# Performance work log

Measured on AMD Instinct MI355X. Metric: run time of the kernel, lower is better.

## Reference

```python
import jax, jax.numpy as jnp
import numpy as np

N_NODES = 100000
N_EDGES = 1600000
IN_F = 32
D = 128
OUT = 16


def setup_inputs() -> dict:
    key = jax.random.key(0)
    ks = jax.random.split(key, 12)
    inp = {
        "x": jax.random.normal(ks[0], (N_NODES, IN_F), dtype=jnp.float32),
        "edge_index": jax.random.randint(ks[1], (2, N_EDGES), 0, N_NODES, dtype=jnp.int64),
        # node embedder (Linear IN_F -> D)
        "W_emb": jax.random.normal(ks[2], (IN_F, D), dtype=jnp.float32) / np.sqrt(IN_F),
        "b_emb": jnp.zeros((D,), dtype=jnp.float32),
        # conv1: relation weight, root weight, bias
        "W1_rel": jax.random.normal(ks[3], (D, D), dtype=jnp.float32) / np.sqrt(D),
        "W1_root": jax.random.normal(ks[4], (D, D), dtype=jnp.float32) / np.sqrt(D),
        "b1": jnp.zeros((D,), dtype=jnp.float32),
        # conv2
        "W2_rel": jax.random.normal(ks[5], (D, D), dtype=jnp.float32) / np.sqrt(D),
        "W2_root": jax.random.normal(ks[6], (D, D), dtype=jnp.float32) / np.sqrt(D),
        "b2": jnp.zeros((D,), dtype=jnp.float32),
        # final layer D -> OUT
        "W_out": jax.random.normal(ks[7], (D, OUT), dtype=jnp.float32) / np.sqrt(D),
        "b_out": jnp.zeros((OUT,), dtype=jnp.float32),
    }
    return inp


def _rgcn_mean(h, src, dst, W_rel, W_root, b):
    # FastRGCNConv with num_relations=1, aggr='mean':
    # out_i = mean_{j -> i}(h_j @ W_rel) + h_i @ W_root + b
    msg = h[src] @ W_rel  # [E, D] gather + per-edge transform
    agg = jax.ops.segment_sum(msg, dst, num_segments=N_NODES)
    cnt = jax.ops.segment_sum(jnp.ones((dst.shape[0],), dtype=h.dtype), dst,
                              num_segments=N_NODES)
    agg = agg / jnp.maximum(cnt, 1.0)[:, None]  # scatter-mean; isolated nodes -> 0
    return agg + h @ W_root + b


def reference(x, edge_index, W_emb, b_emb, W1_rel, W1_root, b1,
              W2_rel, W2_root, b2, W_out, b_out):
    src, dst = edge_index[0], edge_index[1]
    h = x @ W_emb + b_emb                                   # node embed
    h = jax.nn.relu(_rgcn_mean(h, src, dst, W1_rel, W1_root, b1))
    h = jax.nn.relu(_rgcn_mean(h, src, dst, W2_rel, W2_root, b2))
    return h @ W_out + b_out                                # [N_NODES, OUT]
```

## Files before the change

### kernel.cpp

```cpp
#include <hip/hip_runtime.h>
#include <hip/hip_bf16.h>

#define N_NODES 100000
#define N_EDGES 1600000
#define IN_F    32
#define D       128
#define OUT_F   16
#define NB      ((N_NODES + 255) / 256)
#define NSLICE  8
#define SLICE_NODES (N_NODES / NSLICE)
#define FILL_CHUNKS 512

typedef __attribute__((ext_vector_type(8))) short  bf16x8;
typedef __attribute__((ext_vector_type(4))) float  f32x4;

__device__ __forceinline__ unsigned short f2bf(float x) {
    unsigned u = __float_as_uint(x);
    unsigned r = (u + 0x7FFFu + ((u >> 16) & 1u)) >> 16;
    return (unsigned short)r;
}
__device__ __forceinline__ float bf2f(unsigned short h) {
    return __uint_as_float(((unsigned)h) << 16);
}

__global__ __launch_bounds__(256) void k_embed(const float* __restrict__ x,
                                               const float* __restrict__ W,
                                               const float* __restrict__ b,
                                               unsigned short* __restrict__ h_hi,
                                               unsigned short* __restrict__ h_lo) {
    __shared__ float xs[2][IN_F];
    const int col = threadIdx.x & 127;
    const int ng  = threadIdx.x >> 7;
    const int node = blockIdx.x * 2 + ng;

    if (threadIdx.x < 64) {
        int r = threadIdx.x >> 5, c = threadIdx.x & 31;
        int n2 = blockIdx.x * 2 + r;
        xs[r][c] = (n2 < N_NODES) ? x[(long)n2 * IN_F + c] : 0.f;
    }
    __syncthreads();
    if (node >= N_NODES) return;

    float acc = b[col];
#pragma unroll
    for (int k = 0; k < IN_F; ++k)
        acc += xs[ng][k] * W[k * D + col];
    unsigned short hi = f2bf(acc);
    h_hi[(long)node * D + col] = hi;
    h_lo[(long)node * D + col] = f2bf(acc - bf2f(hi));
}

__global__ __launch_bounds__(256) void k_count(const int* __restrict__ dst,
                                               int* __restrict__ cnt) {
    const int slice = blockIdx.x & (NSLICE - 1);
    const int chunk = blockIdx.x >> 3;
    const int lo = slice * SLICE_NODES;
    const int hi = lo + SLICE_NODES;
    for (int e = chunk * 256 + threadIdx.x; e < N_EDGES; e += FILL_CHUNKS * 256) {
        int d = dst[e];
        if (d >= lo && d < hi) atomicAdd(&cnt[d], 1);
    }
}

__global__ __launch_bounds__(256) void k_scan1(const int* __restrict__ cnt,
                                               int* __restrict__ part,
                                               int* __restrict__ blockSums) {
    __shared__ int s[256];
    int i = blockIdx.x * 256 + threadIdx.x;
    int v = (i < N_NODES) ? cnt[i] : 0;
    s[threadIdx.x] = v;
    __syncthreads();
    for (int off = 1; off < 256; off <<= 1) {
        int x = (threadIdx.x >= off) ? s[threadIdx.x - off] : 0;
        __syncthreads();
        s[threadIdx.x] += x;
        __syncthreads();
    }
    if (i < N_NODES) part[i] = s[threadIdx.x] - v;
    if (threadIdx.x == 255) blockSums[blockIdx.x] = s[255];
}

__global__ __launch_bounds__(512) void k_scan2(int* __restrict__ blockSums) {
    __shared__ int s[512];
    int t = threadIdx.x;
    int v = (t < NB) ? blockSums[t] : 0;
    s[t] = v;
    __syncthreads();
    for (int off = 1; off < 512; off <<= 1) {
        int x = (t >= off) ? s[t - off] : 0;
        __syncthreads();
        s[t] += x;
        __syncthreads();
    }
    if (t < NB) blockSums[t] = s[t] - v;
}

__global__ __launch_bounds__(256) void k_scan3(int* __restrict__ offsets,
                                               const int* __restrict__ blockSums,
                                               int* __restrict__ cursor) {
    int i = blockIdx.x * 256 + threadIdx.x;
    if (i < N_NODES) {
        int o = offsets[i] + blockSums[blockIdx.x];
        offsets[i] = o;
        cursor[i]  = o;
    }
}

__global__ __launch_bounds__(256) void k_fill(const int* __restrict__ src,
                                              const int* __restrict__ dst,
                                              int* __restrict__ cursor,
                                              int* __restrict__ csr) {
    const int slice = blockIdx.x & (NSLICE - 1);
    const int chunk = blockIdx.x >> 3;
    const int lo = slice * SLICE_NODES;
    const int hi = lo + SLICE_NODES;
    for (int e = chunk * 256 + threadIdx.x; e < N_EDGES; e += FILL_CHUNKS * 256) {
        int d = dst[e];
        if (d >= lo && d < hi) {
            int p = atomicAdd(&cursor[d], 1);
            csr[p] = src[e];
        }
    }
}

__global__ __launch_bounds__(256) void k_gather(const unsigned short* __restrict__ h_hi,
                                                const int* __restrict__ csr,
                                                const int* __restrict__ offsets,
                                                const int* __restrict__ cnt,
                                                unsigned short* __restrict__ ag_hi,
                                                unsigned short* __restrict__ ag_lo) {
    const int node = blockIdx.x * 16 + (threadIdx.x >> 4);
    const int q8 = (threadIdx.x & 15) << 3;

    const int beg = offsets[node];
    const int deg = cnt[node];
    const int end = beg + deg;

    float a0[8], a1[8];
#pragma unroll
    for (int j = 0; j < 8; ++j) { a0[j] = 0.f; a1[j] = 0.f; }

    int i = beg;
    for (; i + 3 < end; i += 4) {
        int s0 = csr[i], s1 = csr[i + 1], s2 = csr[i + 2], s3 = csr[i + 3];
        bf16x8 v0 = *reinterpret_cast<const bf16x8*>(h_hi + (long)s0 * D + q8);
        bf16x8 v1 = *reinterpret_cast<const bf16x8*>(h_hi + (long)s1 * D + q8);
        bf16x8 v2 = *reinterpret_cast<const bf16x8*>(h_hi + (long)s2 * D + q8);
        bf16x8 v3 = *reinterpret_cast<const bf16x8*>(h_hi + (long)s3 * D + q8);
#pragma unroll
        for (int j = 0; j < 8; ++j) {
            a0[j] += bf2f((unsigned short)v0[j]) + bf2f((unsigned short)v1[j]);
            a1[j] += bf2f((unsigned short)v2[j]) + bf2f((unsigned short)v3[j]);
        }
    }
    for (; i < end; ++i) {
        int s0 = csr[i];
        bf16x8 v0 = *reinterpret_cast<const bf16x8*>(h_hi + (long)s0 * D + q8);
#pragma unroll
        for (int j = 0; j < 8; ++j) a0[j] += bf2f((unsigned short)v0[j]);
    }

    const float sc = 1.f / fmaxf((float)deg, 1.f);
    unsigned short hh[8], ll[8];
#pragma unroll
    for (int j = 0; j < 8; ++j) {
        float v = (a0[j] + a1[j]) * sc;
        unsigned short h = f2bf(v);
        hh[j] = h;
        ll[j] = f2bf(v - bf2f(h));
    }
    *reinterpret_cast<bf16x8*>(ag_hi + (long)node * D + q8) = *reinterpret_cast<bf16x8*>(hh);
    *reinterpret_cast<bf16x8*>(ag_lo + (long)node * D + q8) = *reinterpret_cast<bf16x8*>(ll);
}

__global__ __launch_bounds__(256) void k_wprep(const float* __restrict__ W1r,
                                               const float* __restrict__ W1o,
                                               const float* __restrict__ W2r,
                                               const float* __restrict__ W2o,
                                               unsigned short* __restrict__ wp) {
    int c = blockIdx.x * 256 + threadIdx.x;
    int layer = c >> 12;
    int ko = (c >> 7) & 31;
    int n = c & 127;
    const float* Wrel  = layer ? W2r : W1r;
    const float* Wroot = layer ? W2o : W1o;

    unsigned short hi[8], lo[8];
#pragma unroll
    for (int j = 0; j < 8; ++j) {
        int k = ko * 8 + j;
        float w = (k < D) ? Wrel[k * D + n] : Wroot[(k - D) * D + n];
        unsigned short h = f2bf(w);
        hi[j] = h;
        lo[j] = f2bf(w - bf2f(h));
    }
    unsigned short* base = wp + layer * 65536 + ((ko * 128 + n) << 3);
    *reinterpret_cast<bf16x8*>(base)         = *reinterpret_cast<bf16x8*>(hi);
    *reinterpret_cast<bf16x8*>(base + 32768) = *reinterpret_cast<bf16x8*>(lo);
}

__global__ __launch_bounds__(256) void k_transform(const unsigned short* __restrict__ agg_hi,
                                                   const unsigned short* __restrict__ agg_lo,
                                                   const unsigned short* __restrict__ hin_hi,
                                                   const unsigned short* __restrict__ hin_lo,
                                                   const unsigned short* __restrict__ Wh,
                                                   const unsigned short* __restrict__ Wl,
                                                   const float* __restrict__ b,
                                                   unsigned short* __restrict__ ho_hi,
                                                   unsigned short* __restrict__ ho_lo) {
    __shared__ unsigned short Ahi[32 * 32 * 8];
    __shared__ unsigned short Alo[32 * 32 * 8];
    const int base = blockIdx.x * 32;

    for (int it = 0; it < 4; ++it) {
        int c  = it * 256 + threadIdx.x;
        int ko = c & 31;
        int row = c >> 5;
        long node = base + row;
        long off = (ko < 16) ? (node * D + ko * 8) : (node * D + (ko - 16) * 8);
        const unsigned short* ph = (ko < 16) ? agg_hi : hin_hi;
        const unsigned short* pl = (ko < 16) ? agg_lo : hin_lo;
        bf16x8 vh = *reinterpret_cast<const bf16x8*>(ph + off);
        bf16x8 vl = *reinterpret_cast<const bf16x8*>(pl + off);
        int byteoff = ((ko * 32 + row) * 16) ^ ((ko & 7) << 4);
        *reinterpret_cast<bf16x8*>(reinterpret_cast<char*>(Ahi) + byteoff) = vh;
        *reinterpret_cast<bf16x8*>(reinterpret_cast<char*>(Alo) + byteoff) = vl;
    }
    __syncthreads();

    const int lane = threadIdx.x & 63;
    const int wid  = threadIdx.x >> 6;
    const int mw = wid & 1;
    const int nw = wid >> 1;
    const int l15 = lane & 15;
    const int l4  = lane >> 4;

    f32x4 acc[4];
#pragma unroll
    for (int ct = 0; ct < 4; ++ct) acc[ct] = (f32x4){0.f, 0.f, 0.f, 0.f};

    const int arow = mw * 16 + l15;

#pragma unroll
    for (int s = 0; s < 8; ++s) {
        const int ks = s * 4 + l4;
        const int abyte = ((ks * 32 + arow) * 16) ^ ((ks & 7) << 4);
        bf16x8 ah = *reinterpret_cast<const bf16x8*>(
                        reinterpret_cast<const char*>(Ahi) + abyte);
        bf16x8 al = *reinterpret_cast<const bf16x8*>(
                        reinterpret_cast<const char*>(Alo) + abyte);
#pragma unroll
        for (int ct = 0; ct < 4; ++ct) {
            const int colb = nw * 64 + ct * 16 + l15;
            const long bidx = ((long)(ks * 128 + colb)) << 3;
            bf16x8 bh = *reinterpret_cast<const bf16x8*>(Wh + bidx);
            bf16x8 bl = *reinterpret_cast<const bf16x8*>(Wl + bidx);
            acc[ct] = __builtin_amdgcn_mfma_f32_16x16x32_bf16(ah, bh, acc[ct], 0, 0, 0);
            acc[ct] = __builtin_amdgcn_mfma_f32_16x16x32_bf16(al, bh, acc[ct], 0, 0, 0);
            acc[ct] = __builtin_amdgcn_mfma_f32_16x16x32_bf16(ah, bl, acc[ct], 0, 0, 0);
        }
    }

#pragma unroll
    for (int ct = 0; ct < 4; ++ct) {
        const int col = nw * 64 + ct * 16 + l15;
        const float bv = b[col];
#pragma unroll
        for (int r = 0; r < 4; ++r) {
            long node = base + mw * 16 + l4 * 4 + r;
            float v = fmaxf(acc[ct][r] + bv, 0.f);
            unsigned short h = f2bf(v);
            ho_hi[node * D + col] = h;
            ho_lo[node * D + col] = f2bf(v - bf2f(h));
        }
    }
}

__global__ __launch_bounds__(256) void k_out(const unsigned short* __restrict__ h_hi,
                                             const unsigned short* __restrict__ h_lo,
                                             const float* __restrict__ W,
                                             const float* __restrict__ b,
                                             float* __restrict__ out) {
    long t = (long)blockIdx.x * 256 + threadIdx.x;
    if (t >= (long)N_NODES * OUT_F) return;
    int n = (int)(t >> 4);
    int o = (int)t & 15;
    const unsigned short* hh = h_hi + (long)n * D;
    const unsigned short* hl = h_lo + (long)n * D;
    float acc = b[o];
#pragma unroll
    for (int k = 0; k < D; k += 8) {
        bf16x8 vh = *reinterpret_cast<const bf16x8*>(hh + k);
        bf16x8 vl = *reinterpret_cast<const bf16x8*>(hl + k);
#pragma unroll
        for (int j = 0; j < 8; ++j) {
            float v = bf2f((unsigned short)vh[j]) + bf2f((unsigned short)vl[j]);
            acc += v * W[(k + j) * OUT_F + o];
        }
    }
    out[t] = acc;
}

extern "C" void kernel_launch(void* const* d_in, const int* in_sizes, int n_in,
                              void* d_out, int out_size, void* d_ws, size_t ws_size,
                              hipStream_t stream) {
    const float* x      = (const float*)d_in[0];
    const int*   edge   = (const int*)d_in[1];
    const float* W_emb  = (const float*)d_in[2];
    const float* b_emb  = (const float*)d_in[3];
    const float* W1_rel = (const float*)d_in[4];
    const float* W1_root= (const float*)d_in[5];
    const float* b1     = (const float*)d_in[6];
    const float* W2_rel = (const float*)d_in[7];
    const float* W2_root= (const float*)d_in[8];
    const float* b2     = (const float*)d_in[9];
    const float* W_out  = (const float*)d_in[10];
    const float* b_out  = (const float*)d_in[11];
    float* out = (float*)d_out;

    const int* src = edge;
    const int* dst = edge + N_EDGES;

    const size_t ND = (size_t)N_NODES * D;

    unsigned short* hA_hi = (unsigned short*)d_ws;
    unsigned short* hA_lo = hA_hi + ND;
    unsigned short* hB_hi = hA_lo + ND;
    unsigned short* hB_lo = hB_hi + ND;
    unsigned short* ag_hi = hB_lo + ND;
    unsigned short* ag_lo = ag_hi + ND;
    int*   cnt     = (int*)(ag_lo + ND);
    int*   offsets = cnt + N_NODES;
    int*   cursor  = offsets + N_NODES;
    int*   bsums   = cursor + N_NODES;
    unsigned short* wpack = (unsigned short*)(bsums + 400);
    int*   csr     = (int*)(wpack + 4 * 32768);

    hipMemsetAsync(cnt, 0, N_NODES * sizeof(int), stream);
    k_count<<<NSLICE * FILL_CHUNKS, 256, 0, stream>>>(dst, cnt);
    k_scan1<<<NB, 256, 0, stream>>>(cnt, offsets, bsums);
    k_scan2<<<1, 512, 0, stream>>>(bsums);
    k_scan3<<<NB, 256, 0, stream>>>(offsets, bsums, cursor);
    k_fill<<<NSLICE * FILL_CHUNKS, 256, 0, stream>>>(src, dst, cursor, csr);
    k_wprep<<<32, 256, 0, stream>>>(W1_rel, W1_root, W2_rel, W2_root, wpack);

    k_embed<<<(N_NODES + 1) / 2, 256, 0, stream>>>(x, W_emb, b_emb, hA_hi, hA_lo);

    k_gather<<<N_NODES / 16, 256, 0, stream>>>(hA_hi, csr, offsets, cnt, ag_hi, ag_lo);
    k_transform<<<N_NODES / 32, 256, 0, stream>>>(ag_hi, ag_lo, hA_hi, hA_lo,
                                                  wpack, wpack + 32768, b1, hB_hi, hB_lo);

    k_gather<<<N_NODES / 16, 256, 0, stream>>>(hB_hi, csr, offsets, cnt, ag_hi, ag_lo);
    k_transform<<<N_NODES / 32, 256, 0, stream>>>(ag_hi, ag_lo, hB_hi, hB_lo,
                                                  wpack + 65536, wpack + 98304, b2, hA_hi, hA_lo);

    k_out<<<((long)N_NODES * OUT_F + 255) / 256, 256, 0, stream>>>(hA_hi, hA_lo, W_out, b_out, out);
}
```

Before: 550.9 us.

## Fuse neighbor gather into transform and final projection into last layer

The separate gather kernel is merged into the MFMA transform kernel, so the mean-aggregated rows go straight into shared memory instead of a round trip through global ag_hi/ag_lo buffers. The last layer also applies the output projection in-kernel from shared memory, which removes the k_out launch and the write and re-read of the final hidden state. The embed kernel is rewritten to handle 16 nodes per block with vectorized loads and stores. The trade-off is that the fused kernel has fewer blocks (N/32 instead of N/16 for the gather part), and the latency of the irregular gather now sits inside the GEMM blocks, which could lower occupancy and overlap.

Measured after the change: 505.0 us. 8.3% less time.

```diff
diff --git a/kernel.cpp b/kernel.cpp
--- a/kernel.cpp
+++ b/kernel.cpp
@@ -28,26 +28,45 @@
                                                const float* __restrict__ b,
                                                unsigned short* __restrict__ h_hi,
                                                unsigned short* __restrict__ h_lo) {
-    __shared__ float xs[2][IN_F];
-    const int col = threadIdx.x & 127;
-    const int ng  = threadIdx.x >> 7;
-    const int node = blockIdx.x * 2 + ng;
-
-    if (threadIdx.x < 64) {
-        int r = threadIdx.x >> 5, c = threadIdx.x & 31;
-        int n2 = blockIdx.x * 2 + r;
-        xs[r][c] = (n2 < N_NODES) ? x[(long)n2 * IN_F + c] : 0.f;
+    __shared__ float xs[16][IN_F];
+    const int base = blockIdx.x * 16;
+
+    if (threadIdx.x < 128) {
+        int r = threadIdx.x >> 3, c4 = (threadIdx.x & 7) << 2;
+        *reinterpret_cast<float4*>(&xs[r][c4]) =
+            *reinterpret_cast<const float4*>(x + (long)(base + r) * IN_F + c4);
     }
     __syncthreads();
-    if (node >= N_NODES) return;
-
-    float acc = b[col];
-#pragma unroll
-    for (int k = 0; k < IN_F; ++k)
-        acc += xs[ng][k] * W[k * D + col];
-    unsigned short hi = f2bf(acc);
-    h_hi[(long)node * D + col] = hi;
-    h_lo[(long)node * D + col] = f2bf(acc - bf2f(hi));
+
+    const int nl   = threadIdx.x >> 4;
+    const int col0 = (threadIdx.x & 15) << 3;
+
+    float acc[8];
+    {
+        float4 b0 = *reinterpret_cast<const float4*>(b + col0);
+        float4 b1 = *reinterpret_cast<const float4*>(b + col0 + 4);
+        acc[0] = b0.x; acc[1] = b0.y; acc[2] = b0.z; acc[3] = b0.w;
+        acc[4] = b1.x; acc[5] = b1.y; acc[6] = b1.z; acc[7] = b1.w;
+    }
+#pragma unroll
+    for (int k = 0; k < IN_F; ++k) {
+        const float xv = xs[nl][k];
+        float4 w0 = *reinterpret_cast<const float4*>(W + k * D + col0);
+        float4 w1 = *reinterpret_cast<const float4*>(W + k * D + col0 + 4);
+        acc[0] += xv * w0.x; acc[1] += xv * w0.y; acc[2] += xv * w0.z; acc[3] += xv * w0.w;
+        acc[4] += xv * w1.x; acc[5] += xv * w1.y; acc[6] += xv * w1.z; acc[7] += xv * w1.w;
+    }
+
+    unsigned short hh[8], ll[8];
+#pragma unroll
+    for (int j = 0; j < 8; ++j) {
+        unsigned short h = f2bf(acc[j]);
+        hh[j] = h;
+        ll[j] = f2bf(acc[j] - bf2f(h));
+    }
+    long off = (long)(base + nl) * D + col0;
+    *reinterpret_cast<bf16x8*>(h_hi + off) = *reinterpret_cast<bf16x8*>(hh);
+    *reinterpret_cast<bf16x8*>(h_lo + off) = *reinterpret_cast<bf16x8*>(ll);
 }
 
 __global__ __launch_bounds__(256) void k_count(const int* __restrict__ dst,
@@ -123,56 +142,6 @@
     }
 }
 
-__global__ __launch_bounds__(256) void k_gather(const unsigned short* __restrict__ h_hi,
-                                                const int* __restrict__ csr,
-                                                const int* __restrict__ offsets,
-                                                const int* __restrict__ cnt,
-                                                unsigned short* __restrict__ ag_hi,
-                                                unsigned short* __restrict__ ag_lo) {
-    const int node = blockIdx.x * 16 + (threadIdx.x >> 4);
-    const int q8 = (threadIdx.x & 15) << 3;
-
-    const int beg = offsets[node];
-    const int deg = cnt[node];
-    const int end = beg + deg;
-
-    float a0[8], a1[8];
-#pragma unroll
-    for (int j = 0; j < 8; ++j) { a0[j] = 0.f; a1[j] = 0.f; }
-
-    int i = beg;
-    for (; i + 3 < end; i += 4) {
-        int s0 = csr[i], s1 = csr[i + 1], s2 = csr[i + 2], s3 = csr[i + 3];
-        bf16x8 v0 = *reinterpret_cast<const bf16x8*>(h_hi + (long)s0 * D + q8);
-        bf16x8 v1 = *reinterpret_cast<const bf16x8*>(h_hi + (long)s1 * D + q8);
-        bf16x8 v2 = *reinterpret_cast<const bf16x8*>(h_hi + (long)s2 * D + q8);
-        bf16x8 v3 = *reinterpret_cast<const bf16x8*>(h_hi + (long)s3 * D + q8);
-#pragma unroll
-        for (int j = 0; j < 8; ++j) {
-            a0[j] += bf2f((unsigned short)v0[j]) + bf2f((unsigned short)v1[j]);
-            a1[j] += bf2f((unsigned short)v2[j]) + bf2f((unsigned short)v3[j]);
-        }
-    }
-    for (; i < end; ++i) {
-        int s0 = csr[i];
-        bf16x8 v0 = *reinterpret_cast<const bf16x8*>(h_hi + (long)s0 * D + q8);
-#pragma unroll
-        for (int j = 0; j < 8; ++j) a0[j] += bf2f((unsigned short)v0[j]);
-    }
-
-    const float sc = 1.f / fmaxf((float)deg, 1.f);
-    unsigned short hh[8], ll[8];
-#pragma unroll
-    for (int j = 0; j < 8; ++j) {
-        float v = (a0[j] + a1[j]) * sc;
-        unsigned short h = f2bf(v);
-        hh[j] = h;
-        ll[j] = f2bf(v - bf2f(h));
-    }
-    *reinterpret_cast<bf16x8*>(ag_hi + (long)node * D + q8) = *reinterpret_cast<bf16x8*>(hh);
-    *reinterpret_cast<bf16x8*>(ag_lo + (long)node * D + q8) = *reinterpret_cast<bf16x8*>(ll);
-}
-
 __global__ __launch_bounds__(256) void k_wprep(const float* __restrict__ W1r,
                                                const float* __restrict__ W1o,
                                                const float* __restrict__ W2r,
@@ -199,37 +168,92 @@
     *reinterpret_cast<bf16x8*>(base + 32768) = *reinterpret_cast<bf16x8*>(lo);
 }
 
-__global__ __launch_bounds__(256) void k_transform(const unsigned short* __restrict__ agg_hi,
-                                                   const unsigned short* __restrict__ agg_lo,
-                                                   const unsigned short* __restrict__ hin_hi,
-                                                   const unsigned short* __restrict__ hin_lo,
-                                                   const unsigned short* __restrict__ Wh,
-                                                   const unsigned short* __restrict__ Wl,
-                                                   const float* __restrict__ b,
-                                                   unsigned short* __restrict__ ho_hi,
-                                                   unsigned short* __restrict__ ho_lo) {
+template <bool LAST>
+__global__ __launch_bounds__(256) void k_fused(const unsigned short* __restrict__ hin_hi,
+                                               const unsigned short* __restrict__ hin_lo,
+                                               const int* __restrict__ csr,
+                                               const int* __restrict__ offsets,
+                                               const int* __restrict__ cnt,
+                                               const unsigned short* __restrict__ Wh,
+                                               const unsigned short* __restrict__ Wl,
+                                               const float* __restrict__ b,
+                                               unsigned short* __restrict__ ho_hi,
+                                               unsigned short* __restrict__ ho_lo,
+                                               const float* __restrict__ Wout,
+                                               const float* __restrict__ bout,
+                                               float* __restrict__ outp) {
     __shared__ unsigned short Ahi[32 * 32 * 8];
     __shared__ unsigned short Alo[32 * 32 * 8];
     const int base = blockIdx.x * 32;
-
-    for (int it = 0; it < 4; ++it) {
-        int c  = it * 256 + threadIdx.x;
-        int ko = c & 31;
-        int row = c >> 5;
-        long node = base + row;
-        long off = (ko < 16) ? (node * D + ko * 8) : (node * D + (ko - 16) * 8);
-        const unsigned short* ph = (ko < 16) ? agg_hi : hin_hi;
-        const unsigned short* pl = (ko < 16) ? agg_lo : hin_lo;
-        bf16x8 vh = *reinterpret_cast<const bf16x8*>(ph + off);
-        bf16x8 vl = *reinterpret_cast<const bf16x8*>(pl + off);
+    const int tid  = threadIdx.x;
+
+    {
+        const int ko = tid & 15;
+        const int q8 = ko << 3;
+        for (int half = 0; half < 2; ++half) {
+            const int row  = half * 16 + (tid >> 4);
+            const int node = base + row;
+            const int beg = offsets[node];
+            const int deg = cnt[node];
+            const int end = beg + deg;
+
+            float a0[8], a1[8];
+#pragma unroll
+            for (int j = 0; j < 8; ++j) { a0[j] = 0.f; a1[j] = 0.f; }
+
+            int i = beg;
+            for (; i + 3 < end; i += 4) {
+                int s0 = csr[i], s1 = csr[i + 1], s2 = csr[i + 2], s3 = csr[i + 3];
+                bf16x8 v0 = *reinterpret_cast<const bf16x8*>(hin_hi + (long)s0 * D + q8);
+                bf16x8 v1 = *reinterpret_cast<const bf16x8*>(hin_hi + (long)s1 * D + q8);
+                bf16x8 v2 = *reinterpret_cast<const bf16x8*>(hin_hi + (long)s2 * D + q8);
+                bf16x8 v3 = *reinterpret_cast<const bf16x8*>(hin_hi + (long)s3 * D + q8);
+#pragma unroll
+                for (int j = 0; j < 8; ++j) {
+                    a0[j] += bf2f((unsigned short)v0[j]) + bf2f((unsigned short)v1[j]);
+                    a1[j] += bf2f((unsigned short)v2[j]) + bf2f((unsigned short)v3[j]);
+                }
+            }
+            for (; i < end; ++i) {
+                int s0 = csr[i];
+                bf16x8 v0 = *reinterpret_cast<const bf16x8*>(hin_hi + (long)s0 * D + q8);
+#pragma unroll
+                for (int j = 0; j < 8; ++j) a0[j] += bf2f((unsigned short)v0[j]);
+            }
+
+            const float sc = 1.f / fmaxf((float)deg, 1.f);
+            unsigned short hh[8], ll[8];
+#pragma unroll
+            for (int j = 0; j < 8; ++j) {
+                float v = (a0[j] + a1[j]) * sc;
+                unsigned short h = f2bf(v);
+                hh[j] = h;
+                ll[j] = f2bf(v - bf2f(h));
+            }
+            const int byteoff = ((ko * 32 + row) * 16) ^ ((ko & 7) << 4);
+            *reinterpret_cast<bf16x8*>(reinterpret_cast<char*>(Ahi) + byteoff) =
+                *reinterpret_cast<bf16x8*>(hh);
+            *reinterpret_cast<bf16x8*>(reinterpret_cast<char*>(Alo) + byteoff) =
+                *reinterpret_cast<bf16x8*>(ll);
+        }
+    }
+
+    for (int it = 0; it < 2; ++it) {
+        int c = it * 256 + tid;
+        int ko16 = c & 15;
+        int row  = c >> 4;
+        long off = (long)(base + row) * D + ko16 * 8;
+        bf16x8 vh = *reinterpret_cast<const bf16x8*>(hin_hi + off);
+        bf16x8 vl = *reinterpret_cast<const bf16x8*>(hin_lo + off);
+        int ko = 16 + ko16;
         int byteoff = ((ko * 32 + row) * 16) ^ ((ko & 7) << 4);
         *reinterpret_cast<bf16x8*>(reinterpret_cast<char*>(Ahi) + byteoff) = vh;
         *reinterpret_cast<bf16x8*>(reinterpret_cast<char*>(Alo) + byteoff) = vl;
     }
     __syncthreads();
 
-    const int lane = threadIdx.x & 63;
-    const int wid  = threadIdx.x >> 6;
+    const int lane = tid & 63;
+    const int wid  = tid >> 6;
     const int mw = wid & 1;
     const int nw = wid >> 1;
     const int l15 = lane & 15;
@@ -261,44 +285,49 @@
         }
     }
 
-#pragma unroll
-    for (int ct = 0; ct < 4; ++ct) {
-        const int col = nw * 64 + ct * 16 + l15;
-        const float bv = b[col];
-#pragma unroll
-        for (int r = 0; r < 4; ++r) {
-            long node = base + mw * 16 + l4 * 4 + r;
-            float v = fmaxf(acc[ct][r] + bv, 0.f);
-            unsigned short h = f2bf(v);
-            ho_hi[node * D + col] = h;
-            ho_lo[node * D + col] = f2bf(v - bf2f(h));
-        }
-    }
-}
-
-__global__ __launch_bounds__(256) void k_out(const unsigned short* __restrict__ h_hi,
-                                             const unsigned short* __restrict__ h_lo,
-                                             const float* __restrict__ W,
-                                             const float* __restrict__ b,
-                                             float* __restrict__ out) {
-    long t = (long)blockIdx.x * 256 + threadIdx.x;
-    if (t >= (long)N_NODES * OUT_F) return;
-    int n = (int)(t >> 4);
-    int o = (int)t & 15;
-    const unsigned short* hh = h_hi + (long)n * D;
-    const unsigned short* hl = h_lo + (long)n * D;
-    float acc = b[o];
-#pragma unroll
-    for (int k = 0; k < D; k += 8) {
-        bf16x8 vh = *reinterpret_cast<const bf16x8*>(hh + k);
-        bf16x8 vl = *reinterpret_cast<const bf16x8*>(hl + k);
-#pragma unroll
-        for (int j = 0; j < 8; ++j) {
-            float v = bf2f((unsigned short)vh[j]) + bf2f((unsigned short)vl[j]);
-            acc += v * W[(k + j) * OUT_F + o];
-        }
-    }
-    out[t] = acc;
+    if (!LAST) {
+#pragma unroll
+        for (int ct = 0; ct < 4; ++ct) {
+            const int col = nw * 64 + ct * 16 + l15;
+            const float bv = b[col];
+#pragma unroll
+            for (int r = 0; r < 4; ++r) {
+                long node = base + mw * 16 + l4 * 4 + r;
+                float v = fmaxf(acc[ct][r] + bv, 0.f);
+                unsigned short h = f2bf(v);
+                ho_hi[node * D + col] = h;
+                ho_lo[node * D + col] = f2bf(v - bf2f(h));
+            }
+        }
+    } else {
+        __syncthreads();
+        float* hsm = reinterpret_cast<float*>(Ahi);
+#pragma unroll
+        for (int ct = 0; ct < 4; ++ct) {
+            const int col = nw * 64 + ct * 16 + l15;
+            const float bv = b[col];
+#pragma unroll
+            for (int r = 0; r < 4; ++r) {
+                int nl = mw * 16 + l4 * 4 + r;
+                hsm[nl * D + ((col + 4 * nl) & 127)] = fmaxf(acc[ct][r] + bv, 0.f);
+            }
+        }
+        __syncthreads();
+
+        const int nl = tid >> 3;
+        const int oo = (tid & 7) << 1;
+        float acc0 = bout[oo];
+        float acc1 = bout[oo + 1];
+#pragma unroll 8
+        for (int k = 0; k < D; ++k) {
+            float hv = hsm[nl * D + ((k + 4 * nl) & 127)];
+            float2 w = *reinterpret_cast<const float2*>(Wout + k * OUT_F + oo);
+            acc0 += hv * w.x;
+            acc1 += hv * w.y;
+        }
+        float2 o2 = make_float2(acc0, acc1);
+        *reinterpret_cast<float2*>(outp + (long)(base + nl) * OUT_F + oo) = o2;
+    }
 }
 
 extern "C" void kernel_launch(void* const* d_in, const int* in_sizes, int n_in,
@@ -327,9 +356,7 @@
     unsigned short* hA_lo = hA_hi + ND;
     unsigned short* hB_hi = hA_lo + ND;
     unsigned short* hB_lo = hB_hi + ND;
-    unsigned short* ag_hi = hB_lo + ND;
-    unsigned short* ag_lo = ag_hi + ND;
-    int*   cnt     = (int*)(ag_lo + ND);
+    int*   cnt     = (int*)(hB_lo + ND);
     int*   offsets = cnt + N_NODES;
     int*   cursor  = offsets + N_NODES;
     int*   bsums   = cursor + N_NODES;
@@ -344,15 +371,13 @@
     k_fill<<<NSLICE * FILL_CHUNKS, 256, 0, stream>>>(src, dst, cursor, csr);
     k_wprep<<<32, 256, 0, stream>>>(W1_rel, W1_root, W2_rel, W2_root, wpack);
 
-    k_embed<<<(N_NODES + 1) / 2, 256, 0, stream>>>(x, W_emb, b_emb, hA_hi, hA_lo);
-
-    k_gather<<<N_NODES / 16, 256, 0, stream>>>(hA_hi, csr, offsets, cnt, ag_hi, ag_lo);
-    k_transform<<<N_NODES / 32, 256, 0, stream>>>(ag_hi, ag_lo, hA_hi, hA_lo,
-                                                  wpack, wpack + 32768, b1, hB_hi, hB_lo);
-
-    k_gather<<<N_NODES / 16, 256, 0, stream>>>(hB_hi, csr, offsets, cnt, ag_hi, ag_lo);
-    k_transform<<<N_NODES / 32, 256, 0, stream>>>(ag_hi, ag_lo, hB_hi, hB_lo,
-                                                  wpack + 65536, wpack + 98304, b2, hA_hi, hA_lo);
-
-    k_out<<<((long)N_NODES * OUT_F + 255) / 256, 256, 0, stream>>>(hA_hi, hA_lo, W_out, b_out, out);
-}
+    k_embed<<<N_NODES / 16, 256, 0, stream>>>(x, W_emb, b_emb, hA_hi, hA_lo);
+
+    k_fused<false><<<N_NODES / 32, 256, 0, stream>>>(
+        hA_hi, hA_lo, csr, offsets, cnt,
+        wpack, wpack + 32768, b1, hB_hi, hB_lo, nullptr, nullptr, nullptr);
+
+    k_fused<true><<<N_NODES / 32, 256, 0, stream>>>(
+        hB_hi, hB_lo, csr, offsets, cnt,
+        wpack + 65536, wpack + 98304, b2, nullptr, nullptr, W_out, b_out, out);
+}
```
